# Kernel optimization log

Hardware: AMD Instinct MI355X
Metric: run time of the kernel (lower is better)

## Reference

```python
import jax, jax.numpy as jnp
import numpy as np

T, B, V, L = 512, 32, 512, 128
NEG = -1e9  # safe -inf surrogate (keeps logaddexp gradients finite)


def setup_inputs() -> dict:
    key = jax.random.key(0)
    k1, k2, k3 = jax.random.split(key, 3)
    log_probs = jax.nn.log_softmax(
        jax.random.normal(k1, (T, B, V), dtype=jnp.float32), axis=-1)
    # ASG transition parameter (init ones in the module; use small noise for a
    # non-degenerate reference). transition[i, j] = score of j -> i.
    transition = 0.1 * jax.random.normal(k2, (V, V), dtype=jnp.float32)
    targets = jax.random.randint(k3, (B, L), 0, V)
    input_lengths = jnp.full((B,), T, dtype=jnp.int32)
    target_lengths = jnp.full((B,), L, dtype=jnp.int32)
    return {"log_probs": log_probs, "transition": transition,
            "targets": targets, "input_lengths": input_lengths,
            "target_lengths": target_lengths}


def _fcc(log_probs, transition, input_lengths):
    """Fully-connected criterion: log-partition over all label paths. [B]"""
    def step(alpha, lp_t):  # alpha, lp_t: [B, V]
        # alpha'[b, i] = lp_t[b, i] + logsumexp_j(alpha[b, j] + trans[i, j])
        alpha = lp_t + jax.nn.logsumexp(
            alpha[:, None, :] + transition[None, :, :], axis=2)
        return alpha, jax.nn.logsumexp(alpha, axis=1)

    a0 = log_probs[0]
    _, tail = jax.lax.scan(step, a0, log_probs[1:])
    scores = jnp.concatenate(
        [jax.nn.logsumexp(a0, axis=1)[None], tail], axis=0)  # [T, B]
    return scores[input_lengths - 1, jnp.arange(scores.shape[1])]


def _fac(log_probs, transition, targets, input_lengths, target_lengths):
    """Forced-alignment criterion: DP constrained to the target label seq. [B]"""
    Tt, Bb, _ = log_probs.shape
    Ll = targets.shape[1]
    trans_self = transition[targets, targets]                    # [B, L] stay
    trans_prev = transition[targets[:, 1:], targets[:, :-1]]     # [B, L-1] advance
    # emit[t, b, s] = log_probs[t, b, targets[b, s]]
    emit = jnp.take_along_axis(
        log_probs, jnp.broadcast_to(targets[None], (Tt, Bb, Ll)), axis=2)

    sel = (target_lengths - 1)[:, None]  # [B, 1]

    def final_of(beta):
        return jnp.take_along_axis(beta, sel, axis=1)[:, 0]

    beta0 = jnp.where(jnp.arange(Ll)[None, :] == 0, emit[0], NEG)  # [B, L]

    def step(beta, em_t):
        stay = beta + trans_self
        move = jnp.concatenate(
            [jnp.full((Bb, 1), NEG, beta.dtype),
             beta[:, :-1] + trans_prev], axis=1)
        beta = em_t + jnp.logaddexp(stay, move)
        return beta, final_of(beta)

    _, tail = jax.lax.scan(step, beta0, emit[1:])
    fins = jnp.concatenate([final_of(beta0)[None], tail], axis=0)  # [T, B]
    return fins[input_lengths - 1, jnp.arange(Bb)]


def reference(log_probs, transition, targets, input_lengths, target_lengths):
    # ASG loss (reduction='none'): FCC - FAC, shape [B]
    fcc = _fcc(log_probs, transition, input_lengths)
    fac = _fac(log_probs, transition, targets, input_lengths, target_lengths)
    return fcc - fac
```

## Files before the change

### kernel.cpp

```cpp
#include <hip/hip_runtime.h>
#include <stdint.h>

#define T_ 512
#define B_ 32
#define V_ 512
#define L_ 128
#define NEGF (-1000000000.0f)

#define SE_Q 69.0f
#define SU_Q 127.0f
#define LOGC 9.078313f

typedef int v4i __attribute__((ext_vector_type(4)));

template <int CTRL>
__device__ __forceinline__ int dppmov(int old_, int src) {
    return __builtin_amdgcn_update_dpp(old_, src, CTRL, 0xF, 0xF, false);
}
__device__ __forceinline__ float wave_max64(float x) {
    int xi = __float_as_int(x);
    x = fmaxf(x, __int_as_float(dppmov<0x111>(xi, xi))); xi = __float_as_int(x);
    x = fmaxf(x, __int_as_float(dppmov<0x112>(xi, xi))); xi = __float_as_int(x);
    x = fmaxf(x, __int_as_float(dppmov<0x114>(xi, xi))); xi = __float_as_int(x);
    x = fmaxf(x, __int_as_float(dppmov<0x118>(xi, xi))); xi = __float_as_int(x);
    x = fmaxf(x, __int_as_float(dppmov<0x142>(xi, xi))); xi = __float_as_int(x);
    x = fmaxf(x, __int_as_float(dppmov<0x143>(xi, xi)));
    return x;
}
__device__ __forceinline__ float wave_sum64(float x) {
    int xi = __float_as_int(x);
    x = x + __int_as_float(dppmov<0x111>(xi, xi)); xi = __float_as_int(x);
    x = x + __int_as_float(dppmov<0x112>(xi, xi)); xi = __float_as_int(x);
    x = x + __int_as_float(dppmov<0x114>(xi, xi)); xi = __float_as_int(x);
    x = x + __int_as_float(dppmov<0x118>(xi, xi)); xi = __float_as_int(x);
    x = x + __int_as_float(dppmov<0x142>(xi, xi)); xi = __float_as_int(x);
    x = x + __int_as_float(dppmov<0x143>(xi, xi));
    return x;
}
__device__ __forceinline__ unsigned fkey(float f) {
    unsigned u = __float_as_uint(f);
    return (u & 0x80000000u) ? ~u : (u | 0x80000000u);
}
__device__ __forceinline__ float funkey(unsigned k) {
    unsigned u = (k & 0x80000000u) ? (k ^ 0x80000000u) : ~k;
    return __uint_as_float(u);
}
__device__ __forceinline__ int sel4(v4i a, int r) {
    int x0 = (r & 1) ? a.y : a.x;
    int x1 = (r & 1) ? a.w : a.z;
    return (r & 2) ? x1 : x0;
}

__global__ void asg_prep(const float* __restrict__ trans, uint32_t* __restrict__ Et) {
    int o = blockIdx.x * blockDim.x + threadIdx.x;
    int d    = o & 3;
    int tid  = (o >> 2) & 511;
    int qreg = o >> 11;
    int tt = qreg >> 3, kt = qreg & 7;
    int w = tid >> 6, lane = tid & 63;
    int q = lane >> 4, n = lane & 15;
    int m  = 64 * w + 16 * tt + n;
    int k0 = 64 * kt + 16 * q + 4 * d;
    const float* tp = trans + (size_t)m * V_ + k0;
    uint32_t q0 = (uint32_t)fminf(127.0f, __expf(tp[0]) * SE_Q + 0.5f);
    uint32_t q1 = (uint32_t)fminf(127.0f, __expf(tp[1]) * SE_Q + 0.5f);
    uint32_t q2 = (uint32_t)fminf(127.0f, __expf(tp[2]) * SE_Q + 0.5f);
    uint32_t q3 = (uint32_t)fminf(127.0f, __expf(tp[3]) * SE_Q + 0.5f);
    Et[(size_t)o] = q0 | (q1 << 8) | (q2 << 16) | (q3 << 24);
}

__global__ __attribute__((amdgpu_flat_work_group_size(512, 512),
                          amdgpu_waves_per_eu(2, 2)))
void asg_main(
    const float* __restrict__ lp, const uint32_t* __restrict__ Et,
    const float* __restrict__ trans, const int* __restrict__ targets,
    const int* __restrict__ ilen, const int* __restrict__ tlen,
    float* __restrict__ fcc_ws, float* __restrict__ fac_ws)
{
    __shared__ float facb[256];
    __shared__ __align__(16) uint32_t u_lds[128];
    __shared__ unsigned mslot[2];
    __shared__ unsigned mslotE;
    __shared__ float sumf;

    const int bb  = blockIdx.x;
    const int tid = threadIdx.x;

    if (bb < B_) {
        const int b    = bb;
        const int lane = tid & 63;
        const int w    = tid >> 6;
        const int q    = lane >> 4;
        const int n    = lane & 15;
        const int tt_o = n >> 2;
        const int rg_o = n & 3;
        const int i    = 64 * w + 16 * tt_o + 4 * q + rg_o;
        const int Tlen = ilen[b];

        uint4 er4[32];
        {
            const uint4* Eq = (const uint4*)Et;
            #pragma unroll
            for (int t8 = 0; t8 < 32; ++t8) er4[t8] = Eq[t8 * 512 + tid];
        }

        float alpha = lp[(size_t)b * V_ + i];
        float lpv   = lp[(size_t)1 * (B_ * V_) + (size_t)b * V_ + i];
        if (tid == 511) { mslot[0] = 0u; mslot[1] = 0u; mslotE = 0u; sumf = 0.0f; }
        __syncthreads();

        for (int t = 1; t < Tlen; ++t) {
            {
                float mx = wave_max64(alpha);
                if (lane == 63) atomicMax(&mslot[(t - 1) & 1], fkey(mx));
            }
            __syncthreads();
            float m = funkey(mslot[(t - 1) & 1]);

            {
                float u = __expf(alpha - m);
                uint32_t qu = (uint32_t)(u * SU_Q + 0.5f);
                int pv = (int)(qu << (8 * (i & 3)));
                pv |= dppmov<0xB1>(pv, pv);
                pv |= dppmov<0x4E>(pv, pv);
                if ((i & 3) == 0) u_lds[i >> 2] = (uint32_t)pv;
            }
            if (tid == 511) mslot[t & 1] = 0u;
            __syncthreads();

            int tn = (t + 1 < Tlen) ? (t + 1) : t;
            float lpv_n = lp[(size_t)tn * (B_ * V_) + (size_t)b * V_ + i];

            uint4 bf[8];
            #pragma unroll
            for (int kt = 0; kt < 8; ++kt)
                bf[kt] = *(const uint4*)((const char*)u_lds + 64 * kt + 16 * q);

            v4i a0, a1, a2, a3;
            {
                v4i z = {0, 0, 0, 0};
                a0 = z; a1 = z; a2 = z; a3 = z;
            }
            #pragma unroll
            for (int kt = 0; kt < 8; ++kt) {
                v4i bv = __builtin_bit_cast(v4i, bf[kt]);
                a0 = __builtin_amdgcn_mfma_i32_16x16x64_i8(
                        __builtin_bit_cast(v4i, er4[0 * 8 + kt]), bv, a0, 0, 0, 0);
                a1 = __builtin_amdgcn_mfma_i32_16x16x64_i8(
                        __builtin_bit_cast(v4i, er4[1 * 8 + kt]), bv, a1, 0, 0, 0);
                a2 = __builtin_amdgcn_mfma_i32_16x16x64_i8(
                        __builtin_bit_cast(v4i, er4[2 * 8 + kt]), bv, a2, 0, 0, 0);
                a3 = __builtin_amdgcn_mfma_i32_16x16x64_i8(
                        __builtin_bit_cast(v4i, er4[3 * 8 + kt]), bv, a3, 0, 0, 0);
            }

            int s0 = sel4(a0, rg_o), s1 = sel4(a1, rg_o);
            int s2 = sel4(a2, rg_o), s3 = sel4(a3, rg_o);
            int y0 = (tt_o & 1) ? s1 : s0;
            int y1 = (tt_o & 1) ? s3 : s2;
            int acc = (tt_o & 2) ? y1 : y0;

            alpha = lpv + (m - LOGC) + __logf((float)acc);
            lpv = lpv_n;
        }

        {
            float mx = wave_max64(alpha);
            if (lane == 63) atomicMax(&mslotE, fkey(mx));
        }
        __syncthreads();
        float m2 = funkey(mslotE);
        {
            float sv = wave_sum64(__expf(alpha - m2));
            if (lane == 63) atomicAdd(&sumf, sv);
        }
        __syncthreads();
        if (tid == 0) fcc_ws[b] = m2 + __logf(sumf);
    } else {
        const int b = bb - B_;
        const int l = tid;
        const bool active = (l < L_);
        const int Tlen = ilen[b];
        const int Llen = tlen[b];

        const int tl  = active ? targets[b * L_ + l] : 0;
        const int tlm = (active && l > 0) ? targets[b * L_ + l - 1] : 0;
        const float ts = active ? trans[(size_t)tl * V_ + tl] : 0.0f;
        const float tp = (active && l > 0) ? trans[(size_t)tl * V_ + tlm] : 0.0f;

        float beta = (l == 0) ? lp[(size_t)b * V_ + tl] : NEGF;
        float em_next = active ? lp[(size_t)1 * (B_ * V_) + (size_t)b * V_ + tl] : 0.0f;

        for (int t = 1; t < Tlen; ++t) {
            float* buf = facb + (t & 1) * L_;
            if (active) buf[l] = beta;
            __syncthreads();
            float prev = (active && l > 0) ? buf[l - 1] : NEGF;
            float em = em_next;
            if (active && t + 1 < Tlen)
                em_next = lp[(size_t)(t + 1) * (B_ * V_) + (size_t)b * V_ + tl];
            if (active) {
                float st = beta + ts;
                float mv = prev + tp;
                float mx = fmaxf(st, mv);
                float mn = fminf(st, mv);
                beta = em + mx + log1pf(__expf(mn - mx));
            }
        }
        if (active && l == Llen - 1) fac_ws[b] = beta;
    }
}

__global__ void asg_combine(const float* __restrict__ fcc_ws,
                            const float* __restrict__ fac_ws,
                            float* __restrict__ out) {
    int i = threadIdx.x;
    if (i < B_) out[i] = fcc_ws[i] - fac_ws[i];
}

extern "C" void kernel_launch(void* const* d_in, const int* in_sizes, int n_in,
                              void* d_out, int out_size, void* d_ws, size_t ws_size,
                              hipStream_t stream) {
    const float* lp      = (const float*)d_in[0];
    const float* trans   = (const float*)d_in[1];
    const int*   targets = (const int*)d_in[2];
    const int*   ilen    = (const int*)d_in[3];
    const int*   tlen    = (const int*)d_in[4];
    float* out = (float*)d_out;

    uint32_t* Et     = (uint32_t*)d_ws;
    float*    fcc_ws = (float*)((char*)d_ws + 65536 * 4);
    float*    fac_ws = fcc_ws + B_;

    hipLaunchKernelGGL(asg_prep, dim3(256), dim3(256), 0, stream, trans, Et);
    hipLaunchKernelGGL(asg_main, dim3(2 * B_), dim3(512), 0, stream,
                       lp, Et, trans, targets, ilen, tlen, fcc_ws, fac_ws);
    hipLaunchKernelGGL(asg_combine, dim3(1), dim3(64), 0, stream, fcc_ws, fac_ws, out);
}
```

Baseline: 584.9 us.

## Batch 16 sequences into MFMA N dimension for FCC recursion

```diff
diff --git a/kernel.cpp b/kernel.cpp
--- a/kernel.cpp
+++ b/kernel.cpp
@@ -27,16 +27,6 @@
     x = fmaxf(x, __int_as_float(dppmov<0x143>(xi, xi)));
     return x;
 }
-__device__ __forceinline__ float wave_sum64(float x) {
-    int xi = __float_as_int(x);
-    x = x + __int_as_float(dppmov<0x111>(xi, xi)); xi = __float_as_int(x);
-    x = x + __int_as_float(dppmov<0x112>(xi, xi)); xi = __float_as_int(x);
-    x = x + __int_as_float(dppmov<0x114>(xi, xi)); xi = __float_as_int(x);
-    x = x + __int_as_float(dppmov<0x118>(xi, xi)); xi = __float_as_int(x);
-    x = x + __int_as_float(dppmov<0x142>(xi, xi)); xi = __float_as_int(x);
-    x = x + __int_as_float(dppmov<0x143>(xi, xi));
-    return x;
-}
 __device__ __forceinline__ unsigned fkey(float f) {
     unsigned u = __float_as_uint(f);
     return (u & 0x80000000u) ? ~u : (u | 0x80000000u);
@@ -44,11 +34,6 @@
 __device__ __forceinline__ float funkey(unsigned k) {
     unsigned u = (k & 0x80000000u) ? (k ^ 0x80000000u) : ~k;
     return __uint_as_float(u);
-}
-__device__ __forceinline__ int sel4(v4i a, int r) {
-    int x0 = (r & 1) ? a.y : a.x;
-    int x1 = (r & 1) ? a.w : a.z;
-    return (r & 2) ? x1 : x0;
 }
 
 __global__ void asg_prep(const float* __restrict__ trans, uint32_t* __restrict__ Et) {
@@ -78,24 +63,24 @@
     float* __restrict__ fcc_ws, float* __restrict__ fac_ws)
 {
     __shared__ float facb[256];
-    __shared__ __align__(16) uint32_t u_lds[128];
-    __shared__ unsigned mslot[2];
-    __shared__ unsigned mslotE;
-    __shared__ float sumf;
+    __shared__ __align__(16) uint32_t u_lds[2048];
+    __shared__ unsigned mslot[2][16];
+    __shared__ unsigned mslotE[16];
+    __shared__ float    sumfv[16];
+    __shared__ int      tmax_sh;
 
     const int bb  = blockIdx.x;
     const int tid = threadIdx.x;
 
-    if (bb < B_) {
-        const int b    = bb;
-        const int lane = tid & 63;
-        const int w    = tid >> 6;
-        const int q    = lane >> 4;
-        const int n    = lane & 15;
-        const int tt_o = n >> 2;
-        const int rg_o = n & 3;
-        const int i    = 64 * w + 16 * tt_o + 4 * q + rg_o;
-        const int Tlen = ilen[b];
+    if (bb < 2) {
+        const int bbase = bb * 16;
+        const int lane  = tid & 63;
+        const int w     = tid >> 6;
+        const int q     = lane >> 4;
+        const int n     = lane & 15;
+        const int bg    = bbase + n;
+        const int myT   = ilen[bg];
+        const int myTm1 = myT - 1;
 
         uint4 er4[32];
         {
@@ -104,46 +89,64 @@
             for (int t8 = 0; t8 < 32; ++t8) er4[t8] = Eq[t8 * 512 + tid];
         }
 
-        float alpha = lp[(size_t)b * V_ + i];
-        float lpv   = lp[(size_t)1 * (B_ * V_) + (size_t)b * V_ + i];
-        if (tid == 511) { mslot[0] = 0u; mslot[1] = 0u; mslotE = 0u; sumf = 0.0f; }
-        __syncthreads();
-
-        for (int t = 1; t < Tlen; ++t) {
+        float alpha[16], fin[16], lpv[16];
+        #pragma unroll
+        for (int tt = 0; tt < 4; ++tt) {
+            float4 v = *(const float4*)(lp + (size_t)bg * V_ + 64 * w + 16 * tt + 4 * q);
+            alpha[4 * tt + 0] = v.x; alpha[4 * tt + 1] = v.y;
+            alpha[4 * tt + 2] = v.z; alpha[4 * tt + 3] = v.w;
+        }
+        #pragma unroll
+        for (int j = 0; j < 16; ++j) fin[j] = alpha[j];
+
+        if (tid < 16) {
+            mslot[0][tid] = 0u; mslot[1][tid] = 0u;
+            mslotE[tid] = 0u; sumfv[tid] = 0.0f;
+        }
+        if (tid == 0) tmax_sh = 0;
+        __syncthreads();
+        {
+            float tmx = wave_max64((float)myT);
+            if (lane == 63) atomicMax(&tmax_sh, (int)tmx);
+        }
+        __syncthreads();
+        const int Tmax = tmax_sh;
+
+        for (int t = 1; t < Tmax; ++t) {
             {
-                float mx = wave_max64(alpha);
-                if (lane == 63) atomicMax(&mslot[(t - 1) & 1], fkey(mx));
+                float mx = alpha[0];
+                #pragma unroll
+                for (int j = 1; j < 16; ++j) mx = fmaxf(mx, alpha[j]);
+                atomicMax(&mslot[(t - 1) & 1][n], fkey(mx));
             }
             __syncthreads();
-            float m = funkey(mslot[(t - 1) & 1]);
-
-            {
-                float u = __expf(alpha - m);
-                uint32_t qu = (uint32_t)(u * SU_Q + 0.5f);
-                int pv = (int)(qu << (8 * (i & 3)));
-                pv |= dppmov<0xB1>(pv, pv);
-                pv |= dppmov<0x4E>(pv, pv);
-                if ((i & 3) == 0) u_lds[i >> 2] = (uint32_t)pv;
-            }
-            if (tid == 511) mslot[t & 1] = 0u;
+            const float m = funkey(mslot[(t - 1) & 1][n]);
+
+            #pragma unroll
+            for (int tt = 0; tt < 4; ++tt) {
+                uint32_t q0 = (uint32_t)(__expf(alpha[4 * tt + 0] - m) * SU_Q + 0.5f);
+                uint32_t q1 = (uint32_t)(__expf(alpha[4 * tt + 1] - m) * SU_Q + 0.5f);
+                uint32_t q2 = (uint32_t)(__expf(alpha[4 * tt + 2] - m) * SU_Q + 0.5f);
+                uint32_t q3 = (uint32_t)(__expf(alpha[4 * tt + 3] - m) * SU_Q + 0.5f);
+                uint32_t pk = q0 | (q1 << 8) | (q2 << 16) | (q3 << 24);
+                u_lds[n * 128 + ((4 * w + tt + 3 * n) & 31) * 4 + q] = pk;
+            }
+            #pragma unroll
+            for (int tt = 0; tt < 4; ++tt) {
+                float4 v = *(const float4*)(lp + (size_t)t * (B_ * V_) +
+                                            (size_t)bg * V_ + 64 * w + 16 * tt + 4 * q);
+                lpv[4 * tt + 0] = v.x; lpv[4 * tt + 1] = v.y;
+                lpv[4 * tt + 2] = v.z; lpv[4 * tt + 3] = v.w;
+            }
+            if (tid < 16) mslot[t & 1][tid] = 0u;
             __syncthreads();
 
-            int tn = (t + 1 < Tlen) ? (t + 1) : t;
-            float lpv_n = lp[(size_t)tn * (B_ * V_) + (size_t)b * V_ + i];
-
-            uint4 bf[8];
-            #pragma unroll
-            for (int kt = 0; kt < 8; ++kt)
-                bf[kt] = *(const uint4*)((const char*)u_lds + 64 * kt + 16 * q);
-
             v4i a0, a1, a2, a3;
-            {
-                v4i z = {0, 0, 0, 0};
-                a0 = z; a1 = z; a2 = z; a3 = z;
-            }
+            { v4i z = {0, 0, 0, 0}; a0 = z; a1 = z; a2 = z; a3 = z; }
             #pragma unroll
             for (int kt = 0; kt < 8; ++kt) {
-                v4i bv = __builtin_bit_cast(v4i, bf[kt]);
+                uint4 bf = *(const uint4*)&u_lds[(n * 32 + ((4 * kt + q + 3 * n) & 31)) * 4];
+                v4i bv = __builtin_bit_cast(v4i, bf);
                 a0 = __builtin_amdgcn_mfma_i32_16x16x64_i8(
                         __builtin_bit_cast(v4i, er4[0 * 8 + kt]), bv, a0, 0, 0, 0);
                 a1 = __builtin_amdgcn_mfma_i32_16x16x64_i8(
@@ -153,31 +156,48 @@
                 a3 = __builtin_amdgcn_mfma_i32_16x16x64_i8(
                         __builtin_bit_cast(v4i, er4[3 * 8 + kt]), bv, a3, 0, 0, 0);
             }
-
-            int s0 = sel4(a0, rg_o), s1 = sel4(a1, rg_o);
-            int s2 = sel4(a2, rg_o), s3 = sel4(a3, rg_o);
-            int y0 = (tt_o & 1) ? s1 : s0;
-            int y1 = (tt_o & 1) ? s3 : s2;
-            int acc = (tt_o & 2) ? y1 : y0;
-
-            alpha = lpv + (m - LOGC) + __logf((float)acc);
-            lpv = lpv_n;
-        }
-
-        {
-            float mx = wave_max64(alpha);
-            if (lane == 63) atomicMax(&mslotE, fkey(mx));
-        }
-        __syncthreads();
-        float m2 = funkey(mslotE);
-        {
-            float sv = wave_sum64(__expf(alpha - m2));
-            if (lane == 63) atomicAdd(&sumf, sv);
-        }
-        __syncthreads();
-        if (tid == 0) fcc_ws[b] = m2 + __logf(sumf);
+            const float mc = m - LOGC;
+            alpha[0]  = lpv[0]  + mc + __logf((float)a0.x);
+            alpha[1]  = lpv[1]  + mc + __logf((float)a0.y);
+            alpha[2]  = lpv[2]  + mc + __logf((float)a0.z);
+            alpha[3]  = lpv[3]  + mc + __logf((float)a0.w);
+            alpha[4]  = lpv[4]  + mc + __logf((float)a1.x);
+            alpha[5]  = lpv[5]  + mc + __logf((float)a1.y);
+            alpha[6]  = lpv[6]  + mc + __logf((float)a1.z);
+            alpha[7]  = lpv[7]  + mc + __logf((float)a1.w);
+            alpha[8]  = lpv[8]  + mc + __logf((float)a2.x);
+            alpha[9]  = lpv[9]  + mc + __logf((float)a2.y);
+            alpha[10] = lpv[10] + mc + __logf((float)a2.z);
+            alpha[11] = lpv[11] + mc + __logf((float)a2.w);
+            alpha[12] = lpv[12] + mc + __logf((float)a3.x);
+            alpha[13] = lpv[13] + mc + __logf((float)a3.y);
+            alpha[14] = lpv[14] + mc + __logf((float)a3.z);
+            alpha[15] = lpv[15] + mc + __logf((float)a3.w);
+
+            const bool lastt = (t == myTm1);
+            #pragma unroll
+            for (int j = 0; j < 16; ++j) fin[j] = lastt ? alpha[j] : fin[j];
+        }
+
+        {
+            float mx = fin[0];
+            #pragma unroll
+            for (int j = 1; j < 16; ++j) mx = fmaxf(mx, fin[j]);
+            atomicMax(&mslotE[n], fkey(mx));
+        }
+        __syncthreads();
+        {
+            float m2 = funkey(mslotE[n]);
+            float s = 0.0f;
+            #pragma unroll
+            for (int j = 0; j < 16; ++j) s += __expf(fin[j] - m2);
+            atomicAdd(&sumfv[n], s);
+        }
+        __syncthreads();
+        if (tid < 16)
+            fcc_ws[bbase + tid] = funkey(mslotE[tid]) + __logf(sumfv[tid]);
     } else {
-        const int b = bb - B_;
+        const int b = bb - 2;
         const int l = tid;
         const bool active = (l < L_);
         const int Tlen = ilen[b];
@@ -233,7 +253,7 @@
     float*    fac_ws = fcc_ws + B_;
 
     hipLaunchKernelGGL(asg_prep, dim3(256), dim3(256), 0, stream, trans, Et);
-    hipLaunchKernelGGL(asg_main, dim3(2 * B_), dim3(512), 0, stream,
+    hipLaunchKernelGGL(asg_main, dim3(2 + B_), dim3(512), 0, stream,
                        lp, Et, trans, targets, ilen, tlen, fcc_ws, fac_ws);
     hipLaunchKernelGGL(asg_combine, dim3(1), dim3(64), 0, stream, fcc_ws, fac_ws, out);
 }
```

New measurement: 1.118 ms. 1.91x slower.

## Pack two batch rows per 1024-thread FCC block sharing int8 MFMA transition tiles

Applied to the files above, without the earlier changes.

```diff
diff --git a/kernel.cpp b/kernel.cpp
--- a/kernel.cpp
+++ b/kernel.cpp
@@ -17,26 +17,6 @@
 __device__ __forceinline__ int dppmov(int old_, int src) {
     return __builtin_amdgcn_update_dpp(old_, src, CTRL, 0xF, 0xF, false);
 }
-__device__ __forceinline__ float wave_max64(float x) {
-    int xi = __float_as_int(x);
-    x = fmaxf(x, __int_as_float(dppmov<0x111>(xi, xi))); xi = __float_as_int(x);
-    x = fmaxf(x, __int_as_float(dppmov<0x112>(xi, xi))); xi = __float_as_int(x);
-    x = fmaxf(x, __int_as_float(dppmov<0x114>(xi, xi))); xi = __float_as_int(x);
-    x = fmaxf(x, __int_as_float(dppmov<0x118>(xi, xi))); xi = __float_as_int(x);
-    x = fmaxf(x, __int_as_float(dppmov<0x142>(xi, xi))); xi = __float_as_int(x);
-    x = fmaxf(x, __int_as_float(dppmov<0x143>(xi, xi)));
-    return x;
-}
-__device__ __forceinline__ float wave_sum64(float x) {
-    int xi = __float_as_int(x);
-    x = x + __int_as_float(dppmov<0x111>(xi, xi)); xi = __float_as_int(x);
-    x = x + __int_as_float(dppmov<0x112>(xi, xi)); xi = __float_as_int(x);
-    x = x + __int_as_float(dppmov<0x114>(xi, xi)); xi = __float_as_int(x);
-    x = x + __int_as_float(dppmov<0x118>(xi, xi)); xi = __float_as_int(x);
-    x = x + __int_as_float(dppmov<0x142>(xi, xi)); xi = __float_as_int(x);
-    x = x + __int_as_float(dppmov<0x143>(xi, xi));
-    return x;
-}
 __device__ __forceinline__ unsigned fkey(float f) {
     unsigned u = __float_as_uint(f);
     return (u & 0x80000000u) ? ~u : (u | 0x80000000u);
@@ -44,6 +24,9 @@
 __device__ __forceinline__ float funkey(unsigned k) {
     unsigned u = (k & 0x80000000u) ? (k ^ 0x80000000u) : ~k;
     return __uint_as_float(u);
+}
+__device__ __forceinline__ float rlf(int vi, int l) {
+    return __int_as_float(__builtin_amdgcn_readlane(vi, l));
 }
 __device__ __forceinline__ int sel4(v4i a, int r) {
     int x0 = (r & 1) ? a.y : a.x;
@@ -54,12 +37,12 @@
 __global__ void asg_prep(const float* __restrict__ trans, uint32_t* __restrict__ Et) {
     int o = blockIdx.x * blockDim.x + threadIdx.x;
     int d    = o & 3;
-    int tid  = (o >> 2) & 511;
-    int qreg = o >> 11;
+    int tid  = (o >> 2) & 1023;
+    int qreg = o >> 12;
     int tt = qreg >> 3, kt = qreg & 7;
     int w = tid >> 6, lane = tid & 63;
     int q = lane >> 4, n = lane & 15;
-    int m  = 64 * w + 16 * tt + n;
+    int m  = 32 * w + 16 * tt + n;
     int k0 = 64 * kt + 16 * q + 4 * d;
     const float* tp = trans + (size_t)m * V_ + k0;
     uint32_t q0 = (uint32_t)fminf(127.0f, __expf(tp[0]) * SE_Q + 0.5f);
@@ -69,8 +52,8 @@
     Et[(size_t)o] = q0 | (q1 << 8) | (q2 << 16) | (q3 << 24);
 }
 
-__global__ __attribute__((amdgpu_flat_work_group_size(512, 512),
-                          amdgpu_waves_per_eu(2, 2)))
+__global__ __attribute__((amdgpu_flat_work_group_size(1024, 1024),
+                          amdgpu_waves_per_eu(4, 4)))
 void asg_main(
     const float* __restrict__ lp, const uint32_t* __restrict__ Et,
     const float* __restrict__ trans, const int* __restrict__ targets,
@@ -78,106 +61,133 @@
     float* __restrict__ fcc_ws, float* __restrict__ fac_ws)
 {
     __shared__ float facb[256];
-    __shared__ __align__(16) uint32_t u_lds[128];
-    __shared__ unsigned mslot[2];
-    __shared__ unsigned mslotE;
-    __shared__ float sumf;
+    __shared__ __align__(16) uint32_t u_lds[256];
+    __shared__ unsigned mslot[2][2];
+    __shared__ unsigned mslotE[2];
+    __shared__ float    sumfv[2];
+    __shared__ int      tmax_sh;
 
     const int bb  = blockIdx.x;
     const int tid = threadIdx.x;
 
-    if (bb < B_) {
-        const int b    = bb;
+    if (bb < 16) {
+        const int f    = bb;
         const int lane = tid & 63;
         const int w    = tid >> 6;
         const int q    = lane >> 4;
         const int n    = lane & 15;
-        const int tt_o = n >> 2;
+        const int bsel = n >> 3;
+        const int bg   = 2 * f + bsel;
+        const int tt_o = (n >> 2) & 1;
         const int rg_o = n & 3;
-        const int i    = 64 * w + 16 * tt_o + 4 * q + rg_o;
-        const int Tlen = ilen[b];
-
-        uint4 er4[32];
+        const int row  = 32 * w + 16 * tt_o + 4 * q + rg_o;
+        const int myT  = ilen[bg];
+
+        uint4 er4[16];
         {
             const uint4* Eq = (const uint4*)Et;
             #pragma unroll
-            for (int t8 = 0; t8 < 32; ++t8) er4[t8] = Eq[t8 * 512 + tid];
-        }
-
-        float alpha = lp[(size_t)b * V_ + i];
-        float lpv   = lp[(size_t)1 * (B_ * V_) + (size_t)b * V_ + i];
-        if (tid == 511) { mslot[0] = 0u; mslot[1] = 0u; mslotE = 0u; sumf = 0.0f; }
-        __syncthreads();
-
-        for (int t = 1; t < Tlen; ++t) {
+            for (int qreg = 0; qreg < 16; ++qreg) er4[qreg] = Eq[qreg * 1024 + tid];
+        }
+
+        float alpha = lp[(size_t)bg * V_ + row];
+
+        if (tid < 2) {
+            mslot[0][tid] = 0u; mslot[1][tid] = 0u;
+            mslotE[tid] = 0u; sumfv[tid] = 0.0f;
+        }
+        if (tid == 0) tmax_sh = 0;
+        __syncthreads();
+        if (lane == 0 || lane == 8) atomicMax(&tmax_sh, myT);
+        __syncthreads();
+        const int Tmax = tmax_sh;
+
+        for (int t = 1; t < Tmax; ++t) {
+            const int buf = (t - 1) & 1;
             {
-                float mx = wave_max64(alpha);
-                if (lane == 63) atomicMax(&mslot[(t - 1) & 1], fkey(mx));
+                float v = alpha;
+                int vi = __float_as_int(v);
+                v = fmaxf(v, __int_as_float(dppmov<0xB1>(vi, vi))); vi = __float_as_int(v);
+                v = fmaxf(v, __int_as_float(dppmov<0x4E>(vi, vi))); vi = __float_as_int(v);
+                v = fmaxf(v, __int_as_float(__builtin_amdgcn_ds_swizzle(vi, 0x101F)));
+                vi = __float_as_int(v);
+                float m0 = fmaxf(fmaxf(rlf(vi, 0), rlf(vi, 16)),
+                                 fmaxf(rlf(vi, 32), rlf(vi, 48)));
+                float m1 = fmaxf(fmaxf(rlf(vi, 8), rlf(vi, 24)),
+                                 fmaxf(rlf(vi, 40), rlf(vi, 56)));
+                if (lane == 0) atomicMax(&mslot[buf][0], fkey(m0));
+                if (lane == 8) atomicMax(&mslot[buf][1], fkey(m1));
             }
             __syncthreads();
-            float m = funkey(mslot[(t - 1) & 1]);
+            const float m = funkey(mslot[buf][bsel]);
 
             {
                 float u = __expf(alpha - m);
                 uint32_t qu = (uint32_t)(u * SU_Q + 0.5f);
-                int pv = (int)(qu << (8 * (i & 3)));
+                int pv = (int)(qu << (8 * rg_o));
                 pv |= dppmov<0xB1>(pv, pv);
                 pv |= dppmov<0x4E>(pv, pv);
-                if ((i & 3) == 0) u_lds[i >> 2] = (uint32_t)pv;
-            }
-            if (tid == 511) mslot[t & 1] = 0u;
+                if (rg_o == 0)
+                    u_lds[bsel * 128 + 8 * w + 4 * tt_o + q] = (uint32_t)pv;
+            }
+            float lpv = lp[(size_t)t * (B_ * V_) + (size_t)bg * V_ + row];
+            if (tid == 0) { mslot[t & 1][0] = 0u; mslot[t & 1][1] = 0u; }
             __syncthreads();
 
-            int tn = (t + 1 < Tlen) ? (t + 1) : t;
-            float lpv_n = lp[(size_t)tn * (B_ * V_) + (size_t)b * V_ + i];
-
-            uint4 bf[8];
-            #pragma unroll
-            for (int kt = 0; kt < 8; ++kt)
-                bf[kt] = *(const uint4*)((const char*)u_lds + 64 * kt + 16 * q);
-
-            v4i a0, a1, a2, a3;
-            {
-                v4i z = {0, 0, 0, 0};
-                a0 = z; a1 = z; a2 = z; a3 = z;
-            }
+            v4i a0, a1;
+            { v4i z = {0, 0, 0, 0}; a0 = z; a1 = z; }
+            const char* ub = (const char*)u_lds + bsel * 512;
             #pragma unroll
             for (int kt = 0; kt < 8; ++kt) {
-                v4i bv = __builtin_bit_cast(v4i, bf[kt]);
+                uint4 bf = *(const uint4*)(ub + 64 * kt + 16 * q);
+                v4i bv = __builtin_bit_cast(v4i, bf);
                 a0 = __builtin_amdgcn_mfma_i32_16x16x64_i8(
                         __builtin_bit_cast(v4i, er4[0 * 8 + kt]), bv, a0, 0, 0, 0);
                 a1 = __builtin_amdgcn_mfma_i32_16x16x64_i8(
                         __builtin_bit_cast(v4i, er4[1 * 8 + kt]), bv, a1, 0, 0, 0);
-                a2 = __builtin_amdgcn_mfma_i32_16x16x64_i8(
-                        __builtin_bit_cast(v4i, er4[2 * 8 + kt]), bv, a2, 0, 0, 0);
-                a3 = __builtin_amdgcn_mfma_i32_16x16x64_i8(
-                        __builtin_bit_cast(v4i, er4[3 * 8 + kt]), bv, a3, 0, 0, 0);
-            }
-
-            int s0 = sel4(a0, rg_o), s1 = sel4(a1, rg_o);
-            int s2 = sel4(a2, rg_o), s3 = sel4(a3, rg_o);
-            int y0 = (tt_o & 1) ? s1 : s0;
-            int y1 = (tt_o & 1) ? s3 : s2;
-            int acc = (tt_o & 2) ? y1 : y0;
-
-            alpha = lpv + (m - LOGC) + __logf((float)acc);
-            lpv = lpv_n;
+            }
+            v4i asel;
+            asel.x = tt_o ? a1.x : a0.x;  asel.y = tt_o ? a1.y : a0.y;
+            asel.z = tt_o ? a1.z : a0.z;  asel.w = tt_o ? a1.w : a0.w;
+            int acc = sel4(asel, rg_o);
+
+            float na = lpv + (m - LOGC) + __logf((float)acc);
+            alpha = (t < myT) ? na : alpha;
         }
 
         {
-            float mx = wave_max64(alpha);
-            if (lane == 63) atomicMax(&mslotE, fkey(mx));
-        }
-        __syncthreads();
-        float m2 = funkey(mslotE);
+            float v = alpha;
+            int vi = __float_as_int(v);
+            v = fmaxf(v, __int_as_float(dppmov<0xB1>(vi, vi))); vi = __float_as_int(v);
+            v = fmaxf(v, __int_as_float(dppmov<0x4E>(vi, vi))); vi = __float_as_int(v);
+            v = fmaxf(v, __int_as_float(__builtin_amdgcn_ds_swizzle(vi, 0x101F)));
+            vi = __float_as_int(v);
+            float m0 = fmaxf(fmaxf(rlf(vi, 0), rlf(vi, 16)),
+                             fmaxf(rlf(vi, 32), rlf(vi, 48)));
+            float m1 = fmaxf(fmaxf(rlf(vi, 8), rlf(vi, 24)),
+                             fmaxf(rlf(vi, 40), rlf(vi, 56)));
+            if (lane == 0) atomicMax(&mslotE[0], fkey(m0));
+            if (lane == 8) atomicMax(&mslotE[1], fkey(m1));
+        }
+        __syncthreads();
         {
-            float sv = wave_sum64(__expf(alpha - m2));
-            if (lane == 63) atomicAdd(&sumf, sv);
-        }
-        __syncthreads();
-        if (tid == 0) fcc_ws[b] = m2 + __logf(sumf);
+            const float m2 = funkey(mslotE[bsel]);
+            float s = __expf(alpha - m2);
+            int si = __float_as_int(s);
+            s = s + __int_as_float(dppmov<0xB1>(si, si)); si = __float_as_int(s);
+            s = s + __int_as_float(dppmov<0x4E>(si, si)); si = __float_as_int(s);
+            s = s + __int_as_float(__builtin_amdgcn_ds_swizzle(si, 0x101F));
+            si = __float_as_int(s);
+            float s0 = rlf(si, 0) + rlf(si, 16) + rlf(si, 32) + rlf(si, 48);
+            float s1 = rlf(si, 8) + rlf(si, 24) + rlf(si, 40) + rlf(si, 56);
+            if (lane == 0) atomicAdd(&sumfv[0], s0);
+            if (lane == 8) atomicAdd(&sumfv[1], s1);
+        }
+        __syncthreads();
+        if (tid == 0) fcc_ws[2 * f]     = funkey(mslotE[0]) + __logf(sumfv[0]);
+        if (tid == 8) fcc_ws[2 * f + 1] = funkey(mslotE[1]) + __logf(sumfv[1]);
     } else {
-        const int b = bb - B_;
+        const int b = bb - 16;
         const int l = tid;
         const bool active = (l < L_);
         const int Tlen = ilen[b];
@@ -233,7 +243,7 @@
     float*    fac_ws = fcc_ws + B_;
 
     hipLaunchKernelGGL(asg_prep, dim3(256), dim3(256), 0, stream, trans, Et);
-    hipLaunchKernelGGL(asg_main, dim3(2 * B_), dim3(512), 0, stream,
+    hipLaunchKernelGGL(asg_main, dim3(16 + B_), dim3(1024), 0, stream,
                        lp, Et, trans, targets, ilen, tlen, fcc_ws, fac_ws);
     hipLaunchKernelGGL(asg_combine, dim3(1), dim3(64), 0, stream, fcc_ws, fac_ws, out);
 }
```

Measured after the change: 719.9 us. 1.23x slower.
